# Kernel optimization log

Hardware: AMD Instinct MI355X
Metric: run time of the kernel (lower is better)

The kernel has to match this reference:

```python
import jax, jax.numpy as jnp
import numpy as np

N = 100000   # nodes
E = 1600000  # edges (avg degree 16)
D_IN = 128
H = 256
D_OUT = 128


def setup_inputs() -> dict:
    key = jax.random.key(0)
    ks = jax.random.split(key, 12)

    def lin_w(k, fan_in, fan_out):
        # torch nn.Linear-style uniform init
        bound = 1.0 / np.sqrt(fan_in)
        return jax.random.uniform(k, (fan_in, fan_out), jnp.float32, -bound, bound)

    return {
        "in_feat": jax.random.normal(ks[0], (N, D_IN), jnp.float32),
        "src": jax.random.randint(ks[1], (E,), 0, N, jnp.int32),
        "dst": jax.random.randint(ks[2], (E,), 0, N, jnp.int32),
        "Wc0": lin_w(ks[3], D_IN, H), "bc0": jnp.zeros((H,), jnp.float32),
        "Wc1": lin_w(ks[4], H, H),    "bc1": jnp.zeros((H,), jnp.float32),
        "Wc2": lin_w(ks[5], H, D_OUT),"bc2": jnp.zeros((D_OUT,), jnp.float32),
        "Wr0": lin_w(ks[6], D_OUT, H),"br0": jnp.zeros((H,), jnp.float32),
        "Wr1": lin_w(ks[7], H, H),    "br1": jnp.zeros((H,), jnp.float32),
        "Wr2": lin_w(ks[8], H, D_IN), "br2": jnp.zeros((D_IN,), jnp.float32),
    }


def _graph_conv(h, src, dst, W, b):
    """DGL GraphConv, norm='both': D_out^{-1/2} A D_in^{-1/2} h W + b."""
    ones = jnp.ones(src.shape[0], h.dtype)
    out_deg = jnp.clip(jax.ops.segment_sum(ones, src, num_segments=N), 1.0)
    in_deg = jnp.clip(jax.ops.segment_sum(ones, dst, num_segments=N), 1.0)
    h = h * (out_deg ** -0.5)[:, None]
    h = h @ W                                    # transform before aggregate
    h = jax.ops.segment_sum(h[src], dst, num_segments=N)  # SpMM aggregation
    return h * (in_deg ** -0.5)[:, None] + b


def reference(in_feat, src, dst, Wc0, bc0, Wc1, bc1, Wc2, bc2,
              Wr0, br0, Wr1, br1, Wr2, br2):
    h = jnp.tanh(_graph_conv(in_feat, src, dst, Wc0, bc0))
    h = jnp.tanh(_graph_conv(h, src, dst, Wc1, bc1))
    h = jax.nn.softmax(_graph_conv(h, src, dst, Wc2, bc2), axis=1)
    r = jnp.tanh(h @ Wr0 + br0)
    r = jnp.tanh(r @ Wr1 + br1)
    r = jax.nn.softmax(r @ Wr2 + br2, axis=1)
    return (h, r)
```

## Files before the change

### kernel.cpp

```cpp
#include <hip/hip_runtime.h>

typedef __attribute__((ext_vector_type(8))) short short8;
typedef __attribute__((ext_vector_type(4))) float f32x4;
typedef __attribute__((ext_vector_type(2))) float f32x2;

__device__ __forceinline__ ushort f2bf(float v) {
    unsigned u = __builtin_bit_cast(unsigned, v);
    unsigned r = (u + 0x7FFFu + ((u >> 16) & 1u)) >> 16;
    return (ushort)r;
}
__device__ __forceinline__ float lo16(unsigned p) { return __builtin_bit_cast(float, p << 16); }
__device__ __forceinline__ float hi16(unsigned p) { return __builtin_bit_cast(float, p & 0xFFFF0000u); }

__device__ __forceinline__ float fast_tanh(float x) {
    float cx = fminf(fmaxf(x, -9.f), 9.f);
    float e = __expf(2.f * cx);
    return (e - 1.f) / (e + 1.f);
}

__device__ __forceinline__ void async16(const void* g, void* l) {
    __builtin_amdgcn_global_load_lds(
        (const __attribute__((address_space(1))) unsigned*)g,
        (__attribute__((address_space(3))) unsigned*)l, 16, 0, 0);
}

#define BSHIFT 9
#define CCHUNK 2048

__global__ __launch_bounds__(256) void bucket_count(const int* __restrict__ src,
        const int* __restrict__ dst, int* __restrict__ gbc , int E) {
    __shared__ int cd[4][256];
    __shared__ int cs[4][256];
    int t = threadIdx.x;
    int wv = t >> 6;
    ((int4*)cd)[t] = make_int4(0, 0, 0, 0);
    ((int4*)cs)[t] = make_int4(0, 0, 0, 0);
    __syncthreads();
    int start = blockIdx.x * CCHUNK;
#pragma unroll
    for (int k = 0; k < 2; ++k) {
        int i = start + (k * 256 + t) * 4;
        if (i + 3 < E) {
            int4 d = *(const int4*)(dst + i);
            int4 s = *(const int4*)(src + i);
            atomicAdd(&cd[wv][d.x >> BSHIFT], 1);
            atomicAdd(&cd[wv][d.y >> BSHIFT], 1);
            atomicAdd(&cd[wv][d.z >> BSHIFT], 1);
            atomicAdd(&cd[wv][d.w >> BSHIFT], 1);
            atomicAdd(&cs[wv][s.x >> BSHIFT], 1);
            atomicAdd(&cs[wv][s.y >> BSHIFT], 1);
            atomicAdd(&cs[wv][s.z >> BSHIFT], 1);
            atomicAdd(&cs[wv][s.w >> BSHIFT], 1);
        } else {
#pragma unroll
            for (int m = 0; m < 4; ++m) {
                int ii = i + m;
                if (ii < E) {
                    atomicAdd(&cd[wv][dst[ii] >> BSHIFT], 1);
                    atomicAdd(&cs[wv][src[ii] >> BSHIFT], 1);
                }
            }
        }
    }
    __syncthreads();
    int sd = cd[0][t] + cd[1][t] + cd[2][t] + cd[3][t];
    int ssum = cs[0][t] + cs[1][t] + cs[2][t] + cs[3][t];
    if (sd) atomicAdd(&gbc[t], sd);
    if (ssum) atomicAdd(&gbc[256 + t], ssum);
}

__global__ void scan_buckets(const int* __restrict__ gbc, int* __restrict__ bucketBase,
                             int* __restrict__ pairCursor, int* __restrict__ srcBase,
                             int* __restrict__ srcCursor, int* __restrict__ roff,
                             int N, int E) {
    __shared__ int s[256];
    int t = threadIdx.x;
    int v = gbc[t];
    s[t] = v; __syncthreads();
    for (int o = 1; o < 256; o <<= 1) {
        int y = (t >= o) ? s[t - o] : 0;
        __syncthreads();
        s[t] += y;
        __syncthreads();
    }
    bucketBase[t] = s[t] - v;
    pairCursor[t] = s[t] - v;
    if (t == 255) bucketBase[256] = s[255];
    __syncthreads();
    int v2 = gbc[256 + t];
    s[t] = v2; __syncthreads();
    for (int o = 1; o < 256; o <<= 1) {
        int y = (t >= o) ? s[t - o] : 0;
        __syncthreads();
        s[t] += y;
        __syncthreads();
    }
    srcBase[t] = s[t] - v2;
    srcCursor[t] = s[t] - v2;
    if (t == 255) srcBase[256] = s[255];
    if (t == 0) roff[N] = E;
}

__global__ __launch_bounds__(256) void part_scatter(const int* __restrict__ src,
        const int* __restrict__ dst, int* __restrict__ pairCursor,
        int* __restrict__ srcCursor, uint2* __restrict__ pairs,
        int* __restrict__ sbuf, int E) {
    __shared__ int cntd[256], based[256];
    __shared__ int cnts[256], bases[256];
    int t = threadIdx.x;
    cntd[t] = 0; cnts[t] = 0;
    __syncthreads();
    int start = blockIdx.x * CCHUNK;
    int dd[8], sv[8], rkd[8], rks[8];
#pragma unroll
    for (int k = 0; k < 2; ++k) {
        int i = start + (k * 256 + t) * 4;
        if (i + 3 < E) {
            int4 d = *(const int4*)(dst + i);
            int4 s = *(const int4*)(src + i);
            dd[4 * k + 0] = d.x; dd[4 * k + 1] = d.y; dd[4 * k + 2] = d.z; dd[4 * k + 3] = d.w;
            sv[4 * k + 0] = s.x; sv[4 * k + 1] = s.y; sv[4 * k + 2] = s.z; sv[4 * k + 3] = s.w;
        } else {
#pragma unroll
            for (int m = 0; m < 4; ++m) {
                int ii = i + m;
                if (ii < E) { dd[4 * k + m] = dst[ii]; sv[4 * k + m] = src[ii]; }
                else        { dd[4 * k + m] = -1; sv[4 * k + m] = 0; }
            }
        }
    }
#pragma unroll
    for (int e = 0; e < 8; ++e) {
        if (dd[e] >= 0) {
            rkd[e] = atomicAdd(&cntd[dd[e] >> BSHIFT], 1);
            rks[e] = atomicAdd(&cnts[sv[e] >> BSHIFT], 1);
        }
    }
    __syncthreads();
    based[t] = cntd[t] ? atomicAdd(&pairCursor[t], cntd[t]) : 0;
    bases[t] = cnts[t] ? atomicAdd(&srcCursor[t], cnts[t]) : 0;
    __syncthreads();
#pragma unroll
    for (int e = 0; e < 8; ++e) {
        if (dd[e] >= 0) {
            pairs[based[dd[e] >> BSHIFT] + rkd[e]] = make_uint2((unsigned)sv[e], (unsigned)dd[e]);
            sbuf[bases[sv[e] >> BSHIFT] + rks[e]] = sv[e];
        }
    }
}

__global__ __launch_bounds__(256) void src_count(const int* __restrict__ sbuf,
        const int* __restrict__ srcBase, float* __restrict__ sOut, int N) {
    __shared__ int cnt[512];
    int b = blockIdx.x;
    int t = threadIdx.x;
    int lo = b << BSHIFT;
    int s0 = srcBase[b], s1 = srcBase[b + 1];
    cnt[t] = 0; cnt[t + 256] = 0;
    __syncthreads();
    for (int j = s0 + t; j < s1; j += 256)
        atomicAdd(&cnt[sbuf[j] - lo], 1);
    __syncthreads();
    int n0 = lo + 2 * t, n1 = n0 + 1;
    if (n0 < N) { int c = cnt[2 * t];     sOut[n0] = rsqrtf((float)(c > 0 ? c : 1)); }
    if (n1 < N) { int c = cnt[2 * t + 1]; sOut[n1] = rsqrtf((float)(c > 0 ? c : 1)); }
}

__global__ __launch_bounds__(1024) void build_bucket(const uint2* __restrict__ pairs,
        const int* __restrict__ bucketBase, int* __restrict__ roff,
        float* __restrict__ sIn, int* __restrict__ csr, int N) {
    __shared__ int cnt[512];
    __shared__ int cur[512];
    __shared__ int ss[256];
    int b = blockIdx.x;
    int t = threadIdx.x;
    int lo = b << BSHIFT;
    int s0 = bucketBase[b], s1 = bucketBase[b + 1];
    if (t < 512) cnt[t] = 0;
    __syncthreads();
    for (int j = s0 + t; j < s1; j += 1024)
        atomicAdd(&cnt[pairs[j].y - lo], 1);
    __syncthreads();
    int c0 = 0, c1 = 0;
    if (t < 256) { c0 = cnt[2 * t]; c1 = cnt[2 * t + 1]; ss[t] = c0 + c1; }
    __syncthreads();
    for (int o = 1; o < 256; o <<= 1) {
        int y = 0;
        if (t < 256 && t >= o) y = ss[t - o];
        __syncthreads();
        if (t < 256) ss[t] += y;
        __syncthreads();
    }
    if (t < 256) {
        int eb = ss[t] - (c0 + c1);
        int p0 = s0 + eb, p1 = s0 + eb + c0;
        cur[2 * t] = p0; cur[2 * t + 1] = p1;
        int n0 = lo + 2 * t, n1 = n0 + 1;
        if (n0 < N) { roff[n0] = p0; sIn[n0] = rsqrtf((float)(c0 > 0 ? c0 : 1)); }
        if (n1 < N) { roff[n1] = p1; sIn[n1] = rsqrtf((float)(c1 > 0 ? c1 : 1)); }
    }
    __syncthreads();
    for (int j = s0 + t; j < s1; j += 1024) {
        uint2 p = pairs[j];
        int pos = atomicAdd(&cur[p.y - lo], 1);
        csr[pos] = (int)p.x;
    }
}

__global__ void convw(const float* w0, const float* w1, const float* w2,
                      const float* w3, const float* w4, const float* w5,
                      ushort* __restrict__ Wt) {
    int i = blockIdx.x * 256 + threadIdx.x;
    int base, Km, Nm; const float* W;
    if      (i < 32768)  { base = 0;      Km = 128; Nm = 256; W = w0; }
    else if (i < 98304)  { base = 32768;  Km = 256; Nm = 256; W = w1; }
    else if (i < 131072) { base = 98304;  Km = 256; Nm = 128; W = w2; }
    else if (i < 163840) { base = 131072; Km = 128; Nm = 256; W = w3; }
    else if (i < 229376) { base = 163840; Km = 256; Nm = 256; W = w4; }
    else                 { base = 229376; Km = 256; Nm = 128; W = w5; }
    int l = i - base;
    int k = l / Nm, n = l % Nm;
    Wt[base + n * Km + k] = f2bf(W[l]);
}

__global__ void prescale(const float* __restrict__ x, const float* __restrict__ sOut,
                         unsigned char* __restrict__ o, int total ) {
    int i = blockIdx.x * 256 + threadIdx.x;
    if (i >= total) return;
    int row = i >> 5;
    float s = sOut[row];
    float4 v = ((const float4*)x)[i];
    int pk = __builtin_amdgcn_cvt_pk_fp8_f32(v.x * s, v.y * s, 0, false);
    pk = __builtin_amdgcn_cvt_pk_fp8_f32(v.z * s, v.w * s, pk, true);
    ((unsigned*)o)[i] = (unsigned)pk;
}

__global__ __launch_bounds__(256) void agg128f8(const unsigned char* __restrict__ F,
        const int* __restrict__ csr, const int* __restrict__ roff,
        const float* __restrict__ sIn, ushort* __restrict__ out, int N) {
    int w = blockIdx.x * 4 + (threadIdx.x >> 6);
    if (w >= N) return;
    int lane = threadIdx.x & 63;
    int b = roff[w], e = roff[w + 1];
    int deg = e - b;
    int n = deg < 64 ? deg : 64;
    float a0 = 0.f, a1 = 0.f;
    const char* base = (const char*)F + lane * 2;
    int voff = 0;
    if (n > 0) voff = csr[b + (lane < n ? lane : n - 1)] << 7;
    int j = 0;
    for (; j + 16 <= n; j += 16) {
        unsigned p[16];
#pragma unroll
        for (int k = 0; k < 16; ++k) {
            int o = __shfl(voff, j + k, 64);
            p[k] = *(const ushort*)(base + (size_t)(unsigned)o);
        }
#pragma unroll
        for (int k = 0; k < 16; ++k) {
            f32x2 d = __builtin_amdgcn_cvt_pk_f32_fp8(p[k], false);
            a0 += d.x; a1 += d.y;
        }
    }
    for (; j + 8 <= n; j += 8) {
        unsigned p[8];
#pragma unroll
        for (int k = 0; k < 8; ++k) {
            int o = __shfl(voff, j + k, 64);
            p[k] = *(const ushort*)(base + (size_t)(unsigned)o);
        }
#pragma unroll
        for (int k = 0; k < 8; ++k) {
            f32x2 d = __builtin_amdgcn_cvt_pk_f32_fp8(p[k], false);
            a0 += d.x; a1 += d.y;
        }
    }
    for (; j < n; ++j) {
        int o = __shfl(voff, j, 64);
        unsigned p = *(const ushort*)(base + (size_t)(unsigned)o);
        f32x2 d = __builtin_amdgcn_cvt_pk_f32_fp8(p, false);
        a0 += d.x; a1 += d.y;
    }
    for (int i = b + 64; i < e; ++i) {
        unsigned p = *(const ushort*)(base + ((size_t)csr[i] << 7));
        f32x2 d = __builtin_amdgcn_cvt_pk_f32_fp8(p, false);
        a0 += d.x; a1 += d.y;
    }
    float s = sIn[w];
    ushort2 o2; o2.x = f2bf(a0 * s); o2.y = f2bf(a1 * s);
    *(ushort2*)(out + (size_t)w * 128 + lane * 2) = o2;
}

__global__ __launch_bounds__(256) void agg256f8(const unsigned char* __restrict__ F,
        const int* __restrict__ csr, const int* __restrict__ roff,
        const float* __restrict__ sIn, ushort* __restrict__ out, int N) {
    int w = blockIdx.x * 4 + (threadIdx.x >> 6);
    if (w >= N) return;
    int lane = threadIdx.x & 63;
    int b = roff[w], e = roff[w + 1];
    int deg = e - b;
    int n = deg < 64 ? deg : 64;
    float a0 = 0.f, a1 = 0.f, a2 = 0.f, a3 = 0.f;
    const char* base = (const char*)F + lane * 4;
    int voff = 0;
    if (n > 0) voff = csr[b + (lane < n ? lane : n - 1)] << 8;
    int j = 0;
    for (; j + 16 <= n; j += 16) {
        unsigned p[16];
#pragma unroll
        for (int k = 0; k < 16; ++k) {
            int o = __shfl(voff, j + k, 64);
            p[k] = *(const unsigned*)(base + (size_t)(unsigned)o);
        }
#pragma unroll
        for (int k = 0; k < 16; ++k) {
            f32x2 lo = __builtin_amdgcn_cvt_pk_f32_fp8(p[k], false);
            f32x2 hi = __builtin_amdgcn_cvt_pk_f32_fp8(p[k], true);
            a0 += lo.x; a1 += lo.y; a2 += hi.x; a3 += hi.y;
        }
    }
    for (; j + 8 <= n; j += 8) {
        unsigned p[8];
#pragma unroll
        for (int k = 0; k < 8; ++k) {
            int o = __shfl(voff, j + k, 64);
            p[k] = *(const unsigned*)(base + (size_t)(unsigned)o);
        }
#pragma unroll
        for (int k = 0; k < 8; ++k) {
            f32x2 lo = __builtin_amdgcn_cvt_pk_f32_fp8(p[k], false);
            f32x2 hi = __builtin_amdgcn_cvt_pk_f32_fp8(p[k], true);
            a0 += lo.x; a1 += lo.y; a2 += hi.x; a3 += hi.y;
        }
    }
    for (; j < n; ++j) {
        int o = __shfl(voff, j, 64);
        unsigned p = *(const unsigned*)(base + (size_t)(unsigned)o);
        f32x2 lo = __builtin_amdgcn_cvt_pk_f32_fp8(p, false);
        f32x2 hi = __builtin_amdgcn_cvt_pk_f32_fp8(p, true);
        a0 += lo.x; a1 += lo.y; a2 += hi.x; a3 += hi.y;
    }
    for (int i = b + 64; i < e; ++i) {
        unsigned p = *(const unsigned*)(base + ((size_t)csr[i] << 8));
        f32x2 lo = __builtin_amdgcn_cvt_pk_f32_fp8(p, false);
        f32x2 hi = __builtin_amdgcn_cvt_pk_f32_fp8(p, true);
        a0 += lo.x; a1 += lo.y; a2 += hi.x; a3 += hi.y;
    }
    float s = sIn[w];
    ushort4 o4;
    o4.x = f2bf(a0 * s); o4.y = f2bf(a1 * s);
    o4.z = f2bf(a2 * s); o4.w = f2bf(a3 * s);
    *(ushort4*)(out + (size_t)w * 256 + lane * 4) = o4;
}

__global__ __launch_bounds__(256) void agg_softmax_f8(const unsigned char* __restrict__ F,
        const int* __restrict__ csr, const int* __restrict__ roff,
        const float* __restrict__ sIn, const float* __restrict__ bias,
        float* __restrict__ outh, ushort* __restrict__ outb, int N) {
    int w = blockIdx.x * 4 + (threadIdx.x >> 6);
    if (w >= N) return;
    int lane = threadIdx.x & 63;
    int b = roff[w], e = roff[w + 1];
    int deg = e - b;
    int n = deg < 64 ? deg : 64;
    float a0 = 0.f, a1 = 0.f;
    const char* base = (const char*)F + lane * 2;
    int voff = 0;
    if (n > 0) voff = csr[b + (lane < n ? lane : n - 1)] << 7;
    int j = 0;
    for (; j + 16 <= n; j += 16) {
        unsigned p[16];
#pragma unroll
        for (int k = 0; k < 16; ++k) {
            int o = __shfl(voff, j + k, 64);
            p[k] = *(const ushort*)(base + (size_t)(unsigned)o);
        }
#pragma unroll
        for (int k = 0; k < 16; ++k) {
            f32x2 d = __builtin_amdgcn_cvt_pk_f32_fp8(p[k], false);
            a0 += d.x; a1 += d.y;
        }
    }
    for (; j + 8 <= n; j += 8) {
        unsigned p[8];
#pragma unroll
        for (int k = 0; k < 8; ++k) {
            int o = __shfl(voff, j + k, 64);
            p[k] = *(const ushort*)(base + (size_t)(unsigned)o);
        }
#pragma unroll
        for (int k = 0; k < 8; ++k) {
            f32x2 d = __builtin_amdgcn_cvt_pk_f32_fp8(p[k], false);
            a0 += d.x; a1 += d.y;
        }
    }
    for (; j < n; ++j) {
        int o = __shfl(voff, j, 64);
        unsigned p = *(const ushort*)(base + (size_t)(unsigned)o);
        f32x2 d = __builtin_amdgcn_cvt_pk_f32_fp8(p, false);
        a0 += d.x; a1 += d.y;
    }
    for (int i = b + 64; i < e; ++i) {
        unsigned p = *(const ushort*)(base + ((size_t)csr[i] << 7));
        f32x2 d = __builtin_amdgcn_cvt_pk_f32_fp8(p, false);
        a0 += d.x; a1 += d.y;
    }
    float s = sIn[w];
    float2 bb = *(const float2*)(bias + lane * 2);
    float l0 = a0 * s + bb.x, l1 = a1 * s + bb.y;
    float m = fmaxf(l0, l1);
    for (int o = 32; o; o >>= 1) m = fmaxf(m, __shfl_xor(m, o, 64));
    float e0 = __expf(l0 - m), e1 = __expf(l1 - m);
    float sm = e0 + e1;
    for (int o = 32; o; o >>= 1) sm += __shfl_xor(sm, o, 64);
    float inv = 1.f / sm;
    float r0 = e0 * inv, r1 = e1 * inv;
    float2 fo; fo.x = r0; fo.y = r1;
    *(float2*)(outh + (size_t)w * 128 + lane * 2) = fo;
    ushort2 o2; o2.x = f2bf(r0); o2.y = f2bf(r1);
    *(ushort2*)(outb + (size_t)w * 128 + lane * 2) = o2;
}

template <int MODE, int K>
__global__ __launch_bounds__(256) void gemm2(
        const ushort* __restrict__ A, const ushort* __restrict__ Wt,
        const float* __restrict__ bias, const float* __restrict__ rowscale,
        void* __restrict__ out, int M, int Nn) {
    constexpr int SLOTS = K / 8;
    constexpr int KS = K / 32;
    constexpr int RPI = 1024 / (2 * K);
    __shared__ ushort ldsW[128 * K];

    const int tid = threadIdx.x;
    const int lane = tid & 63;
    const int wid = tid >> 6;
    const int nby = Nn >> 7;
    const int bx = (int)blockIdx.x / nby;
    const int by = (int)blockIdx.x - bx * nby;
    const int rowbase = bx * 128;
    const int colbase = by * 128;

#pragma unroll
    for (int it = 0; it < 128 / (4 * RPI); ++it) {
        int row0 = it * (4 * RPI) + wid * RPI;
        int rl = row0 + lane / SLOTS;
        int sl = lane % SLOTS;
        int gs = sl ^ (rl & 7);
        async16(Wt + (size_t)(colbase + rl) * K + gs * 8,
                (char*)ldsW + row0 * (2 * K));
    }

    const int l15 = lane & 15, l4 = lane >> 4;
    short8 a[2][KS];
#pragma unroll
    for (int rt = 0; rt < 2; ++rt) {
        int grow = rowbase + wid * 32 + rt * 16 + l15;
        if (grow > M - 1) grow = M - 1;
        const ushort* ap = A + (size_t)grow * K + l4 * 8;
#pragma unroll
        for (int ks = 0; ks < KS; ++ks)
            a[rt][ks] = *(const short8*)(ap + ks * 32);
    }

    f32x4 acc[2][8];
#pragma unroll
    for (int i = 0; i < 2; ++i)
#pragma unroll
        for (int j = 0; j < 8; ++j) acc[i][j] = (f32x4){0.f, 0.f, 0.f, 0.f};

    __syncthreads();

#pragma unroll
    for (int ks = 0; ks < KS; ++ks) {
        short8 b[8];
#pragma unroll
        for (int ct = 0; ct < 8; ++ct) {
            int n = ct * 16 + l15;
            int slot = (ks * 4 + l4) ^ (n & 7);
            b[ct] = *(const short8*)&ldsW[n * K + slot * 8];
        }
#pragma unroll
        for (int ct = 0; ct < 8; ++ct) {
            acc[0][ct] = __builtin_amdgcn_mfma_f32_16x16x32_bf16(a[0][ks], b[ct], acc[0][ct], 0, 0, 0);
            acc[1][ct] = __builtin_amdgcn_mfma_f32_16x16x32_bf16(a[1][ks], b[ct], acc[1][ct], 0, 0, 0);
        }
    }

    float bv[8];
#pragma unroll
    for (int ct = 0; ct < 8; ++ct)
        bv[ct] = (MODE != 1 && MODE != 5 && bias) ? bias[colbase + ct * 16 + l15] : 0.f;

    if (MODE == 4 || MODE == 5) {
#pragma unroll
        for (int rt = 0; rt < 2; ++rt) {
#pragma unroll
            for (int rg = 0; rg < 4; ++rg) {
                int row = rowbase + wid * 32 + rt * 16 + l4 * 4 + rg;
                if (row >= M) continue;
                float sc = (MODE == 4 && rowscale) ? rowscale[row] : 1.f;
#pragma unroll
                for (int ct = 0; ct < 8; ++ct) {
                    float v = acc[rt][ct][rg] + bv[ct];
                    if (MODE == 4) v = fast_tanh(v) * sc;
                    float vp = __shfl_xor(v, 1, 64);
                    if ((l15 & 1) == 0) {
                        int pk = __builtin_amdgcn_cvt_pk_fp8_f32(v, vp, 0, false);
                        *(ushort*)((char*)out + (size_t)row * Nn + colbase + ct * 16 + l15)
                            = (ushort)(pk & 0xFFFF);
                    }
                }
            }
        }
    } else if (MODE != 3) {
#pragma unroll
        for (int rt = 0; rt < 2; ++rt) {
#pragma unroll
            for (int rg = 0; rg < 4; ++rg) {
                int row = rowbase + wid * 32 + rt * 16 + l4 * 4 + rg;
                if (row >= M) continue;
                float sc = 1.f;
                if (MODE == 0 && rowscale) sc = rowscale[row];
#pragma unroll
                for (int ct = 0; ct < 8; ++ct) {
                    int col = colbase + ct * 16 + l15;
                    float v = acc[rt][ct][rg] + bv[ct];
                    if (MODE == 0) v = fast_tanh(v) * sc;
                    ((ushort*)out)[(size_t)row * Nn + col] = f2bf(v);
                }
            }
        }
    } else {
#pragma unroll
        for (int rt = 0; rt < 2; ++rt) {
#pragma unroll
            for (int rg = 0; rg < 4; ++rg) {
                int row = rowbase + wid * 32 + rt * 16 + l4 * 4 + rg;
                float m = acc[rt][0][rg] + bv[0];
#pragma unroll
                for (int ct = 1; ct < 8; ++ct) m = fmaxf(m, acc[rt][ct][rg] + bv[ct]);
                m = fmaxf(m, __shfl_xor(m, 1, 64));
                m = fmaxf(m, __shfl_xor(m, 2, 64));
                m = fmaxf(m, __shfl_xor(m, 4, 64));
                m = fmaxf(m, __shfl_xor(m, 8, 64));
                float ev[8], s = 0.f;
#pragma unroll
                for (int ct = 0; ct < 8; ++ct) {
                    ev[ct] = __expf(acc[rt][ct][rg] + bv[ct] - m);
                    s += ev[ct];
                }
                s += __shfl_xor(s, 1, 64);
                s += __shfl_xor(s, 2, 64);
                s += __shfl_xor(s, 4, 64);
                s += __shfl_xor(s, 8, 64);
                float inv = 1.f / s;
                if (row < M) {
#pragma unroll
                    for (int ct = 0; ct < 8; ++ct) {
                        int col = colbase + ct * 16 + l15;
                        ((float*)out)[(size_t)row * Nn + col] = ev[ct] * inv;
                    }
                }
            }
        }
    }
}

extern "C" void kernel_launch(void* const* d_in, const int* in_sizes, int n_in,
                              void* d_out, int out_size, void* d_ws, size_t ws_size,
                              hipStream_t stream) {
    (void)n_in; (void)out_size; (void)ws_size;
    const float* in_feat = (const float*)d_in[0];
    const int*   src     = (const int*)d_in[1];
    const int*   dstp    = (const int*)d_in[2];
    const float* Wc0 = (const float*)d_in[3];  const float* bc0 = (const float*)d_in[4];
    const float* Wc1 = (const float*)d_in[5];  const float* bc1 = (const float*)d_in[6];
    const float* Wc2 = (const float*)d_in[7];  const float* bc2 = (const float*)d_in[8];
    const float* Wr0 = (const float*)d_in[9];  const float* br0 = (const float*)d_in[10];
    const float* Wr1 = (const float*)d_in[11]; const float* br1 = (const float*)d_in[12];
    const float* Wr2 = (const float*)d_in[13]; const float* br2 = (const float*)d_in[14];

    const int N = in_sizes[0] / 128;
    const int E = in_sizes[1];
    const int numBuckets = (N + ((1 << BSHIFT) - 1)) >> BSHIFT;

    char* ws = (char*)d_ws;
    size_t off = 0;
    auto alloc = [&](size_t bytes) -> char* {
        char* p = ws + off;
        off += (bytes + 255) & ~(size_t)255;
        return p;
    };
    char* S1 = alloc((size_t)N * 256 * 2);
    char* S2 = alloc((size_t)N * 256 * 2);
    int* csr    = (int*)alloc((size_t)E * 4);
    int* roff   = (int*)alloc((size_t)(N + 1) * 4);
    int* sbuf   = (int*)alloc((size_t)E * 4);
    float* sOut = (float*)alloc((size_t)N * 4);
    float* sIn  = (float*)alloc((size_t)N * 4);
    ushort* Wt  = (ushort*)alloc(262144 * 2);
    int* gbc        = (int*)alloc(512 * 4);
    int* bucketBase = (int*)alloc(257 * 4);
    int* pairCursor = (int*)alloc(256 * 4);
    int* srcBase    = (int*)alloc(257 * 4);
    int* srcCursor  = (int*)alloc(256 * 4);
    uint2* pairs = (uint2*)S2;

    hipMemsetAsync(gbc, 0, 512 * 4, stream);

    int nblk = (E + CCHUNK - 1) / CCHUNK;
    bucket_count<<<nblk, 256, 0, stream>>>(src, dstp, gbc, E);
    scan_buckets<<<1, 256, 0, stream>>>(gbc, bucketBase, pairCursor, srcBase, srcCursor,
                                        roff, N, E);
    part_scatter<<<nblk, 256, 0, stream>>>(src, dstp, pairCursor, srcCursor, pairs, sbuf, E);
    build_bucket<<<numBuckets, 1024, 0, stream>>>(pairs, bucketBase, roff, sIn, csr, N);
    src_count<<<numBuckets, 256, 0, stream>>>(sbuf, srcBase, sOut, N);

    convw<<<262144 / 256, 256, 0, stream>>>(Wc0, Wc1, Wc2, Wr0, Wr1, Wr2, Wt);

    unsigned char* Xf8 = (unsigned char*)S1;
    prescale<<<(N * 32 + 255) / 256, 256, 0, stream>>>(in_feat, sOut, Xf8, N * 32);

    int aggGrid = (N + 3) / 4;
    int nrb = (N + 127) / 128;

    ushort* A0 = (ushort*)S2;
    agg128f8<<<aggGrid, 256, 0, stream>>>(Xf8, csr, roff, sIn, A0, N);
    unsigned char* B1f8 = (unsigned char*)S1;
    gemm2<4, 128><<<nrb * 2, 256, 0, stream>>>(A0, Wt, bc0, sOut, B1f8, N, 256);
    ushort* A1 = (ushort*)S2;
    agg256f8<<<aggGrid, 256, 0, stream>>>(B1f8, csr, roff, sIn, A1, N);
    ushort* B2 = (ushort*)S1;
    gemm2<0, 256><<<nrb * 2, 256, 0, stream>>>(A1, Wt + 32768, bc1, sOut, B2, N, 256);
    unsigned char* T3f8 = (unsigned char*)S2;
    gemm2<5, 256><<<nrb, 256, 0, stream>>>(B2, Wt + 98304, nullptr, nullptr, T3f8, N, 128);
    float* outh = (float*)d_out;
    ushort* Hbf = (ushort*)S1;
    agg_softmax_f8<<<aggGrid, 256, 0, stream>>>(T3f8, csr, roff, sIn, bc2, outh, Hbf, N);
    ushort* R1 = (ushort*)S2;
    gemm2<0, 128><<<nrb * 2, 256, 0, stream>>>(Hbf, Wt + 131072, br0, nullptr, R1, N, 256);
    ushort* R2 = (ushort*)S1;
    gemm2<0, 256><<<nrb * 2, 256, 0, stream>>>(R1, Wt + 163840, br1, nullptr, R2, N, 256);
    gemm2<3, 256><<<nrb, 256, 0, stream>>>(R2, Wt + 229376, br2, nullptr,
                                           outh + (size_t)N * 128, N, 128);
}
```

Measured before the change: 694.7 us.

## Restructure GEMM to 8 waves of 16 rows with k-slot-major LDS weight layout

Replaces the 4-wave GEMM, where each wave computed 32 rows, with an 8-wave version where each wave computes 16 rows. This halves per-thread accumulator and A-fragment registers to allow more waves per CU. The LDS weight tile is re-laid out k-slot-major, with each 16-byte slot holding 64 consecutive output columns, so B-fragment reads become contiguous without the XOR swizzle. The cost is that each B fragment read from LDS now feeds one MFMA instead of two, doubling LDS read traffic per MFMA.

```diff
diff --git a/kernel.cpp b/kernel.cpp
--- a/kernel.cpp
+++ b/kernel.cpp
@@ -422,14 +422,12 @@
 }
 
 template <int MODE, int K>
-__global__ __launch_bounds__(256) void gemm2(
+__global__ __launch_bounds__(512, 4) void gemm3(
         const ushort* __restrict__ A, const ushort* __restrict__ Wt,
         const float* __restrict__ bias, const float* __restrict__ rowscale,
         void* __restrict__ out, int M, int Nn) {
-    constexpr int SLOTS = K / 8;
     constexpr int KS = K / 32;
-    constexpr int RPI = 1024 / (2 * K);
-    __shared__ ushort ldsW[128 * K];
+    __shared__ ushort ldsW[(K / 8) * 1024];
 
     const int tid = threadIdx.x;
     const int lane = tid & 63;
@@ -441,48 +439,37 @@
     const int colbase = by * 128;
 
 #pragma unroll
-    for (int it = 0; it < 128 / (4 * RPI); ++it) {
-        int row0 = it * (4 * RPI) + wid * RPI;
-        int rl = row0 + lane / SLOTS;
-        int sl = lane % SLOTS;
-        int gs = sl ^ (rl & 7);
-        async16(Wt + (size_t)(colbase + rl) * K + gs * 8,
-                (char*)ldsW + row0 * (2 * K));
+    for (int it = 0; it < KS; ++it) {
+        int c = wid * KS + it;
+        int s = c >> 1, h = c & 1;
+        async16(Wt + (size_t)(colbase + h * 64 + lane) * K + s * 8,
+                (char*)ldsW + c * 1024);
     }
 
     const int l15 = lane & 15, l4 = lane >> 4;
-    short8 a[2][KS];
-#pragma unroll
-    for (int rt = 0; rt < 2; ++rt) {
-        int grow = rowbase + wid * 32 + rt * 16 + l15;
+    short8 a[KS];
+    {
+        int grow = rowbase + wid * 16 + l15;
         if (grow > M - 1) grow = M - 1;
         const ushort* ap = A + (size_t)grow * K + l4 * 8;
 #pragma unroll
         for (int ks = 0; ks < KS; ++ks)
-            a[rt][ks] = *(const short8*)(ap + ks * 32);
-    }
-
-    f32x4 acc[2][8];
-#pragma unroll
-    for (int i = 0; i < 2; ++i)
-#pragma unroll
-        for (int j = 0; j < 8; ++j) acc[i][j] = (f32x4){0.f, 0.f, 0.f, 0.f};
+            a[ks] = *(const short8*)(ap + ks * 32);
+    }
+
+    f32x4 acc[8];
+#pragma unroll
+    for (int j = 0; j < 8; ++j) acc[j] = (f32x4){0.f, 0.f, 0.f, 0.f};
 
     __syncthreads();
 
 #pragma unroll
     for (int ks = 0; ks < KS; ++ks) {
-        short8 b[8];
+        const ushort* bp = &ldsW[(ks * 4 + l4) * 1024 + l15 * 8];
 #pragma unroll
         for (int ct = 0; ct < 8; ++ct) {
-            int n = ct * 16 + l15;
-            int slot = (ks * 4 + l4) ^ (n & 7);
-            b[ct] = *(const short8*)&ldsW[n * K + slot * 8];
-        }
-#pragma unroll
-        for (int ct = 0; ct < 8; ++ct) {
-            acc[0][ct] = __builtin_amdgcn_mfma_f32_16x16x32_bf16(a[0][ks], b[ct], acc[0][ct], 0, 0, 0);
-            acc[1][ct] = __builtin_amdgcn_mfma_f32_16x16x32_bf16(a[1][ks], b[ct], acc[1][ct], 0, 0, 0);
+            short8 b = *(const short8*)(bp + ct * 128);
+            acc[ct] = __builtin_amdgcn_mfma_f32_16x16x32_bf16(a[ks], b, acc[ct], 0, 0, 0);
         }
     }
 
@@ -493,73 +480,64 @@
 
     if (MODE == 4 || MODE == 5) {
 #pragma unroll
-        for (int rt = 0; rt < 2; ++rt) {
-#pragma unroll
-            for (int rg = 0; rg < 4; ++rg) {
-                int row = rowbase + wid * 32 + rt * 16 + l4 * 4 + rg;
-                if (row >= M) continue;
-                float sc = (MODE == 4 && rowscale) ? rowscale[row] : 1.f;
-#pragma unroll
-                for (int ct = 0; ct < 8; ++ct) {
-                    float v = acc[rt][ct][rg] + bv[ct];
-                    if (MODE == 4) v = fast_tanh(v) * sc;
-                    float vp = __shfl_xor(v, 1, 64);
-                    if ((l15 & 1) == 0) {
-                        int pk = __builtin_amdgcn_cvt_pk_fp8_f32(v, vp, 0, false);
-                        *(ushort*)((char*)out + (size_t)row * Nn + colbase + ct * 16 + l15)
-                            = (ushort)(pk & 0xFFFF);
-                    }
+        for (int rg = 0; rg < 4; ++rg) {
+            int row = rowbase + wid * 16 + l4 * 4 + rg;
+            if (row >= M) continue;
+            float sc = (MODE == 4 && rowscale) ? rowscale[row] : 1.f;
+#pragma unroll
+            for (int ct = 0; ct < 8; ++ct) {
+                float v = acc[ct][rg] + bv[ct];
+                if (MODE == 4) v = fast_tanh(v) * sc;
+                float vp = __shfl_xor(v, 1, 64);
+                if ((l15 & 1) == 0) {
+                    int pk = __builtin_amdgcn_cvt_pk_fp8_f32(v, vp, 0, false);
+                    *(ushort*)((char*)out + (size_t)row * Nn + colbase + ct * 16 + l15)
+                        = (ushort)(pk & 0xFFFF);
                 }
             }
         }
     } else if (MODE != 3) {
 #pragma unroll
-        for (int rt = 0; rt < 2; ++rt) {
-#pragma unroll
-            for (int rg = 0; rg < 4; ++rg) {
-                int row = rowbase + wid * 32 + rt * 16 + l4 * 4 + rg;
-                if (row >= M) continue;
-                float sc = 1.f;
-                if (MODE == 0 && rowscale) sc = rowscale[row];
+        for (int rg = 0; rg < 4; ++rg) {
+            int row = rowbase + wid * 16 + l4 * 4 + rg;
+            if (row >= M) continue;
+            float sc = 1.f;
+            if (MODE == 0 && rowscale) sc = rowscale[row];
+#pragma unroll
+            for (int ct = 0; ct < 8; ++ct) {
+                int col = colbase + ct * 16 + l15;
+                float v = acc[ct][rg] + bv[ct];
+                if (MODE == 0) v = fast_tanh(v) * sc;
+                ((ushort*)out)[(size_t)row * Nn + col] = f2bf(v);
+            }
+        }
+    } else {
+#pragma unroll
+        for (int rg = 0; rg < 4; ++rg) {
+            int row = rowbase + wid * 16 + l4 * 4 + rg;
+            float m = acc[0][rg] + bv[0];
+#pragma unroll
+            for (int ct = 1; ct < 8; ++ct) m = fmaxf(m, acc[ct][rg] + bv[ct]);
+            m = fmaxf(m, __shfl_xor(m, 1, 64));
+            m = fmaxf(m, __shfl_xor(m, 2, 64));
+            m = fmaxf(m, __shfl_xor(m, 4, 64));
+            m = fmaxf(m, __shfl_xor(m, 8, 64));
+            float ev[8], s = 0.f;
+#pragma unroll
+            for (int ct = 0; ct < 8; ++ct) {
+                ev[ct] = __expf(acc[ct][rg] + bv[ct] - m);
+                s += ev[ct];
+            }
+            s += __shfl_xor(s, 1, 64);
+            s += __shfl_xor(s, 2, 64);
+            s += __shfl_xor(s, 4, 64);
+            s += __shfl_xor(s, 8, 64);
+            float inv = 1.f / s;
+            if (row < M) {
 #pragma unroll
                 for (int ct = 0; ct < 8; ++ct) {
                     int col = colbase + ct * 16 + l15;
-                    float v = acc[rt][ct][rg] + bv[ct];
-                    if (MODE == 0) v = fast_tanh(v) * sc;
-                    ((ushort*)out)[(size_t)row * Nn + col] = f2bf(v);
-                }
-            }
-        }
-    } else {
-#pragma unroll
-        for (int rt = 0; rt < 2; ++rt) {
-#pragma unroll
-            for (int rg = 0; rg < 4; ++rg) {
-                int row = rowbase + wid * 32 + rt * 16 + l4 * 4 + rg;
-                float m = acc[rt][0][rg] + bv[0];
-#pragma unroll
-                for (int ct = 1; ct < 8; ++ct) m = fmaxf(m, acc[rt][ct][rg] + bv[ct]);
-                m = fmaxf(m, __shfl_xor(m, 1, 64));
-                m = fmaxf(m, __shfl_xor(m, 2, 64));
-                m = fmaxf(m, __shfl_xor(m, 4, 64));
-                m = fmaxf(m, __shfl_xor(m, 8, 64));
-                float ev[8], s = 0.f;
-#pragma unroll
-                for (int ct = 0; ct < 8; ++ct) {
-                    ev[ct] = __expf(acc[rt][ct][rg] + bv[ct] - m);
-                    s += ev[ct];
-                }
-                s += __shfl_xor(s, 1, 64);
-                s += __shfl_xor(s, 2, 64);
-                s += __shfl_xor(s, 4, 64);
-                s += __shfl_xor(s, 8, 64);
-                float inv = 1.f / s;
-                if (row < M) {
-#pragma unroll
-                    for (int ct = 0; ct < 8; ++ct) {
-                        int col = colbase + ct * 16 + l15;
-                        ((float*)out)[(size_t)row * Nn + col] = ev[ct] * inv;
-                    }
+                    ((float*)out)[(size_t)row * Nn + col] = ev[ct] * inv;
                 }
             }
         }
@@ -627,20 +605,20 @@
     ushort* A0 = (ushort*)S2;
     agg128f8<<<aggGrid, 256, 0, stream>>>(Xf8, csr, roff, sIn, A0, N);
     unsigned char* B1f8 = (unsigned char*)S1;
-    gemm2<4, 128><<<nrb * 2, 256, 0, stream>>>(A0, Wt, bc0, sOut, B1f8, N, 256);
+    gemm3<4, 128><<<nrb * 2, 512, 0, stream>>>(A0, Wt, bc0, sOut, B1f8, N, 256);
     ushort* A1 = (ushort*)S2;
     agg256f8<<<aggGrid, 256, 0, stream>>>(B1f8, csr, roff, sIn, A1, N);
     ushort* B2 = (ushort*)S1;
-    gemm2<0, 256><<<nrb * 2, 256, 0, stream>>>(A1, Wt + 32768, bc1, sOut, B2, N, 256);
+    gemm3<0, 256><<<nrb * 2, 512, 0, stream>>>(A1, Wt + 32768, bc1, sOut, B2, N, 256);
     unsigned char* T3f8 = (unsigned char*)S2;
-    gemm2<5, 256><<<nrb, 256, 0, stream>>>(B2, Wt + 98304, nullptr, nullptr, T3f8, N, 128);
+    gemm3<5, 256><<<nrb, 512, 0, stream>>>(B2, Wt + 98304, nullptr, nullptr, T3f8, N, 128);
     float* outh = (float*)d_out;
     ushort* Hbf = (ushort*)S1;
     agg_softmax_f8<<<aggGrid, 256, 0, stream>>>(T3f8, csr, roff, sIn, bc2, outh, Hbf, N);
     ushort* R1 = (ushort*)S2;
-    gemm2<0, 128><<<nrb * 2, 256, 0, stream>>>(Hbf, Wt + 131072, br0, nullptr, R1, N, 256);
+    gemm3<0, 128><<<nrb * 2, 512, 0, stream>>>(Hbf, Wt + 131072, br0, nullptr, R1, N, 256);
     ushort* R2 = (ushort*)S1;
-    gemm2<0, 256><<<nrb * 2, 256, 0, stream>>>(R1, Wt + 163840, br1, nullptr, R2, N, 256);
-    gemm2<3, 256><<<nrb, 256, 0, stream>>>(R2, Wt + 229376, br2, nullptr,
+    gemm3<0, 256><<<nrb * 2, 512, 0, stream>>>(R1, Wt + 163840, br1, nullptr, R2, N, 256);
+    gemm3<3, 256><<<nrb, 512, 0, stream>>>(R2, Wt + 229376, br2, nullptr,
                                            outh + (size_t)N * 128, N, 128);
 }
```

Result: faster. 643.1 us (median of 2 runs) (-7.4%).
